# Optimization experiments

Measured on AMD Instinct MI355X. Metric: run time of the kernel, lower is better.

Reference implementation:

```python
import jax, jax.numpy as jnp
import numpy as np

B, S, HID, H, DH = 8, 4096, 1024, 16, 64


def setup_inputs() -> dict:
    key = jax.random.key(0)
    ks = jax.random.split(key, 5)
    return {
        "hidden_states": jax.random.normal(ks[0], (B, S, HID), dtype=jnp.float32),
        "attention_mask": jnp.ones((B, 1, 1, S), dtype=jnp.float32),
        "Wq": jax.random.normal(ks[1], (HID, HID), dtype=jnp.float32) * (HID ** -0.5),
        "Wk": jax.random.normal(ks[2], (HID, HID), dtype=jnp.float32) * (HID ** -0.5),
        "Wv": jax.random.normal(ks[3], (HID, HID), dtype=jnp.float32) * (HID ** -0.5),
        "att_weight": jax.random.normal(ks[4], (H, 1, DH), dtype=jnp.float32) * (DH ** -0.5),
    }


def _heads(x):
    # [B,S,HID] -> [B,H,S,DH]
    b, s, _ = x.shape
    return x.reshape(b, s, H, DH).transpose(0, 2, 1, 3)


def reference(hidden_states, attention_mask, Wq, Wk, Wv, att_weight):
    # bias-free projections (torch Linear: x @ W.T)
    q = _heads(hidden_states @ Wq.T)  # [B,H,S,DH]
    k = _heads(hidden_states @ Wk.T)
    v = _heads(hidden_states @ Wv.T)

    mask = attention_mask.transpose(0, 1, 3, 2)  # [B,1,S,1]
    aw = att_weight[:, 0, :]  # [H,DH]

    q_scores = jnp.einsum('bhsd,hd->bhs', q, aw)[..., None] * mask  # [B,H,S,1]
    k_scores = jnp.einsum('bhsd,hd->bhs', k, aw)[..., None] * mask  # [B,H,S,1]

    length = jnp.sum(mask, axis=-2, keepdims=True)            # [B,1,1,1]
    mean_value = jnp.sum(v * mask, axis=-2, keepdims=True)    # [B,H,1,DH]

    query_values = q_scores * mean_value                      # [B,H,S,DH] outer product
    key_values = jnp.einsum('bhs,bhsd->bhd', k_scores[..., 0], v)[:, :, None, :]  # [B,H,1,DH]

    ctx = (query_values + key_values) / length                # [B,H,S,DH]
    ctx = ctx.transpose(0, 2, 1, 3).reshape(ctx.shape[0], ctx.shape[2], H * DH)
    return ctx
```

## Files before the change

kernel.cpp:

```cpp
#include <hip/hip_runtime.h>

#define BB 8
#define SS 4096
#define HIDD 1024
#define HH 16
#define DHH 64

typedef __attribute__((ext_vector_type(8))) short bf16x8;
typedef __attribute__((ext_vector_type(4))) float f32x4;

static __device__ __forceinline__ unsigned short f2bf(float x) {
    union { float f; unsigned int u; } a; a.f = x;
    unsigned int r = a.u + 0x7FFFu + ((a.u >> 16) & 1u);
    return (unsigned short)(r >> 16);
}
static __device__ __forceinline__ float bf2f(unsigned short b) {
    union { unsigned int u; float f; } a; a.u = ((unsigned int)b) << 16;
    return a.f;
}

__global__ __launch_bounds__(256) void k_prep(const float* __restrict__ Wq,
                                              const float* __restrict__ Wk,
                                              const float* __restrict__ aw,
                                              unsigned short* __restrict__ bpack) {
    int k = blockIdx.x * 256 + threadIdx.x;
    int h = blockIdx.y;
    const float* W = blockIdx.z ? Wk : Wq;
    int nt = blockIdx.z;
    float acc = 0.f;
#pragma unroll
    for (int d = 0; d < DHH; ++d) {
        acc += aw[h * DHH + d] * W[(size_t)(h * DHH + d) * HIDD + k];
    }
    unsigned short hi = f2bf(acc);
    unsigned short lo = f2bf(acc - bf2f(hi));
    int kk   = k >> 5;
    int r5   = (k >> 3) & 3;
    int j    = k & 7;
    int lane = r5 * 16 + h;
    size_t baseh = ((size_t)(kk * 4 + 0 + nt) * 256 + lane * 4) * 2 + j;
    size_t basel = ((size_t)(kk * 4 + 2 + nt) * 256 + lane * 4) * 2 + j;
    bpack[baseh] = hi;
    bpack[basel] = lo;
}

#define KC 64
__global__ __launch_bounds__(256) void k_scores(const float* __restrict__ hid,
                                                const float* __restrict__ mask,
                                                const unsigned short* __restrict__ bpack,
                                                float* __restrict__ qsb,
                                                float* __restrict__ ksb) {
    __shared__ float shh[2][64 * 68];

    const int t    = threadIdx.x;
    const int lane = t & 63;
    const int wave = t >> 6;
    const int rbase = blockIdx.x * 64;
    const size_t gbase = (size_t)rbase * HIDD;

    int srow[5], scol[5];
#pragma unroll
    for (int j = 0; j < 5; ++j) {
        int f = (j < 4) ? (j * 256 + t) : (1024 + t);
        int r = f / 17;
        int c = f - r * 17;
        srow[j] = r;
        scol[j] = (c == 16) ? 0 : c;
    }
    const bool extra = (t < 64);

    auto stage = [&](int chunk, int buf) {
#pragma unroll
        for (int j = 0; j < 4; ++j) {
            const float* gp = hid + gbase + (size_t)srow[j] * HIDD
                              + chunk * KC + scol[j] * 4;
            float* lp = &shh[buf][(j * 256 + t) * 4];
            __builtin_amdgcn_global_load_lds(
                (const __attribute__((address_space(1))) void*)gp,
                (__attribute__((address_space(3))) void*)lp, 16, 0, 0);
        }
        if (extra) {
            const float* gp = hid + gbase + (size_t)srow[4] * HIDD
                              + chunk * KC + scol[4] * 4;
            float* lp = &shh[buf][(1024 + t) * 4];
            __builtin_amdgcn_global_load_lds(
                (const __attribute__((address_space(1))) void*)gp,
                (__attribute__((address_space(3))) void*)lp, 16, 0, 0);
        }
    };

    const bf16x8* bview = reinterpret_cast<const bf16x8*>(bpack);
    const int mrow = wave * 16 + (lane & 15);
    const int koff = (lane >> 4) * 8;

    f32x4 accq = {0.f, 0.f, 0.f, 0.f};
    f32x4 acck = {0.f, 0.f, 0.f, 0.f};

    stage(0, 0);

    for (int chunk = 0; chunk < HIDD / KC; ++chunk) {
        const int buf = chunk & 1;
        asm volatile("s_waitcnt vmcnt(0)" ::: "memory");
        __syncthreads();
        if (chunk + 1 < HIDD / KC) stage(chunk + 1, buf ^ 1);

#pragma unroll
        for (int kl = 0; kl < 2; ++kl) {
            const int kk = chunk * 2 + kl;
            bf16x8 bh0 = bview[(kk * 4 + 0) * 64 + lane];
            bf16x8 bh1 = bview[(kk * 4 + 1) * 64 + lane];
            bf16x8 bl0 = bview[(kk * 4 + 2) * 64 + lane];
            bf16x8 bl1 = bview[(kk * 4 + 3) * 64 + lane];

            const float* ap = &shh[buf][mrow * 68 + kl * 32 + koff];
            float4 av0 = *reinterpret_cast<const float4*>(ap);
            float4 av1 = *reinterpret_cast<const float4*>(ap + 4);
            float a[8] = {av0.x, av0.y, av0.z, av0.w, av1.x, av1.y, av1.z, av1.w};
            union { bf16x8 v; unsigned short u[8]; } Ahi, Alo;
#pragma unroll
            for (int j = 0; j < 8; ++j) {
                unsigned short hb = f2bf(a[j]);
                Ahi.u[j] = hb;
                Alo.u[j] = f2bf(a[j] - bf2f(hb));
            }

            accq = __builtin_amdgcn_mfma_f32_16x16x32_bf16(Ahi.v, bh0, accq, 0, 0, 0);
            accq = __builtin_amdgcn_mfma_f32_16x16x32_bf16(Alo.v, bh0, accq, 0, 0, 0);
            accq = __builtin_amdgcn_mfma_f32_16x16x32_bf16(Ahi.v, bl0, accq, 0, 0, 0);
            acck = __builtin_amdgcn_mfma_f32_16x16x32_bf16(Ahi.v, bh1, acck, 0, 0, 0);
            acck = __builtin_amdgcn_mfma_f32_16x16x32_bf16(Alo.v, bh1, acck, 0, 0, 0);
            acck = __builtin_amdgcn_mfma_f32_16x16x32_bf16(Ahi.v, bl1, acck, 0, 0, 0);
        }
    }

#pragma unroll
    for (int reg = 0; reg < 4; ++reg) {
        int grow = rbase + wave * 16 + (lane >> 4) * 4 + reg;
        float m = mask[grow];
        qsb[(size_t)grow * 16 + (lane & 15)] = accq[reg] * m;
        ksb[(size_t)grow * 20 + (lane & 15)] = acck[reg] * m;
        if ((lane & 15) == 0) ksb[(size_t)grow * 20 + 16] = m;
    }
}

__global__ __launch_bounds__(256) void k_ksh(const float* __restrict__ hid,
                                             const float* __restrict__ ksb,
                                             float* __restrict__ part) {
    int b  = blockIdx.y;
    int i  = threadIdx.x * 4;
    int s0 = blockIdx.x * 64;

    float4 acc[17];
#pragma unroll
    for (int c = 0; c < 17; ++c) acc[c] = make_float4(0.f, 0.f, 0.f, 0.f);

    const float* hb = hid + (size_t)(b * SS + s0) * HIDD + i;
    const float* sb = ksb + (size_t)(b * SS + s0) * 20;

#pragma unroll 4
    for (int s = 0; s < 64; ++s) {
        float4 hv = *reinterpret_cast<const float4*>(hb + (size_t)s * HIDD);
        const float* sc = sb + s * 20;
#pragma unroll
        for (int c = 0; c < 17; ++c) {
            float scv = sc[c];
            acc[c].x += scv * hv.x;
            acc[c].y += scv * hv.y;
            acc[c].z += scv * hv.z;
            acc[c].w += scv * hv.w;
        }
    }

    float* pb = part + (((size_t)blockIdx.x * 8 + b) * 17) * 1024 + i;
#pragma unroll
    for (int c = 0; c < 17; ++c) {
        *reinterpret_cast<float4*>(pb + c * 1024) = acc[c];
    }
}

__global__ __launch_bounds__(256) void k_red(const float* __restrict__ part,
                                             float* __restrict__ ksh,
                                             float* __restrict__ hsum) {
    int gid = blockIdx.x * 256 + threadIdx.x;
    int b = gid / 17408;
    int r = gid - b * 17408;
    int c = r >> 10;
    int i = r & 1023;

    float s = 0.f;
#pragma unroll 8
    for (int k = 0; k < 64; ++k)
        s += part[(((size_t)k * 8 + b) * 17 + c) * 1024 + i];

    if (c < 16) ksh[((size_t)b * 16 + c) * 1024 + i] = s;
    else        hsum[b * 1024 + i] = s;
}

__global__ __launch_bounds__(256) void k_fin(const float* __restrict__ Wv,
                                             const float* __restrict__ mask,
                                             const float* __restrict__ hsum,
                                             const float* __restrict__ ksh,
                                             float* __restrict__ mvn,
                                             float* __restrict__ kvn) {
    int b  = blockIdx.x;
    int j  = blockIdx.y * 32 + (threadIdx.x >> 3);
    int sl = threadIdx.x & 7;

    __shared__ float red[256];
    float lsum = 0.f;
    for (int s = threadIdx.x; s < SS; s += 256) lsum += mask[b * SS + s];
    red[threadIdx.x] = lsum;
    __syncthreads();
    for (int off = 128; off; off >>= 1) {
        if (threadIdx.x < off) red[threadIdx.x] += red[threadIdx.x + off];
        __syncthreads();
    }
    float invlen = 1.0f / red[0];

    int h = j >> 6;
    const float4* w4 = reinterpret_cast<const float4*>(Wv + (size_t)j * HIDD + sl * 128);
    const float4* hv = reinterpret_cast<const float4*>(hsum + b * HIDD + sl * 128);
    const float4* kv = reinterpret_cast<const float4*>(ksh + ((size_t)b * 16 + h) * HIDD + sl * 128);

    float mv = 0.f, kvv = 0.f;
#pragma unroll
    for (int c = 0; c < 32; ++c) {
        float4 w = w4[c], a = hv[c], k2 = kv[c];
        mv  += w.x * a.x  + w.y * a.y  + w.z * a.z  + w.w * a.w;
        kvv += w.x * k2.x + w.y * k2.y + w.z * k2.z + w.w * k2.w;
    }
#pragma unroll
    for (int off = 1; off < 8; off <<= 1) {
        mv  += __shfl_xor(mv, off);
        kvv += __shfl_xor(kvv, off);
    }
    if (sl == 0) {
        mvn[b * HIDD + j] = mv * invlen;
        kvn[b * HIDD + j] = kvv * invlen;
    }
}

__global__ __launch_bounds__(256) void k_out(const float* __restrict__ qsb,
                                             const float* __restrict__ mvn,
                                             const float* __restrict__ kvn,
                                             float* __restrict__ outp) {
    size_t e0 = ((size_t)blockIdx.x * 256 + threadIdx.x) * 8;
    int b   = (int)(e0 >> 22);
    int rem = (int)(e0 & ((1u << 22) - 1));
    int s   = rem >> 10;
    int j   = rem & 1023;

    float q = qsb[(size_t)(b * SS + s) * 16 + (j >> 6)];
    const float4* mv4 = reinterpret_cast<const float4*>(mvn + b * HIDD + j);
    const float4* kv4 = reinterpret_cast<const float4*>(kvn + b * HIDD + j);
    float4 m0 = mv4[0], m1 = mv4[1];
    float4 k0 = kv4[0], k1 = kv4[1];

    float4 o0, o1;
    o0.x = q * m0.x + k0.x;  o0.y = q * m0.y + k0.y;
    o0.z = q * m0.z + k0.z;  o0.w = q * m0.w + k0.w;
    o1.x = q * m1.x + k1.x;  o1.y = q * m1.y + k1.y;
    o1.z = q * m1.z + k1.z;  o1.w = q * m1.w + k1.w;

    float4* op = reinterpret_cast<float4*>(outp + e0);
    op[0] = o0;
    op[1] = o1;
}

extern "C" void kernel_launch(void* const* d_in, const int* in_sizes, int n_in,
                              void* d_out, int out_size, void* d_ws, size_t ws_size,
                              hipStream_t stream) {
    const float* hid  = (const float*)d_in[0];
    const float* mask = (const float*)d_in[1];
    const float* Wq   = (const float*)d_in[2];
    const float* Wk   = (const float*)d_in[3];
    const float* Wv   = (const float*)d_in[4];
    const float* aw   = (const float*)d_in[5];
    float* outp = (float*)d_out;

    float* ws   = (float*)d_ws;
    unsigned short* bpack = (unsigned short*)ws;
    float* qsb  = ws + 32768;
    float* ksb  = qsb + 524288;
    float* ksh  = ksb + 655360;
    float* hsum = ksh + 131072;
    float* mvn  = hsum + 8192;
    float* kvn  = mvn + 8192;
    float* part = kvn + 8192;

    k_prep  <<<dim3(4, 16, 2), 256, 0, stream>>>(Wq, Wk, aw, bpack);
    k_scores<<<dim3(512),      256, 0, stream>>>(hid, mask, bpack, qsb, ksb);
    k_ksh   <<<dim3(64, 8),    256, 0, stream>>>(hid, ksb, part);
    k_red   <<<dim3(544),      256, 0, stream>>>(part, ksh, hsum);
    k_fin   <<<dim3(8, 32),    256, 0, stream>>>(Wv, mask, hsum, ksh, mvn, kvn);
    k_out   <<<dim3(16384),    256, 0, stream>>>(qsb, mvn, kvn, outp);
}
```

Measured before the change: 349.6 us.

## Triple-buffer hidden-state staging in k_scores with partial vmcnt waits

The LDS staging of hidden-state chunks in k_scores moves from two buffers to three, so two chunks are kept in flight ahead of the compute. The loop waits with vmcnt(5) instead of vmcnt(0), letting the next chunk's loads stay outstanding while the current chunk is consumed. The extra-row loads are remapped so each wave issues them for its own 16 lanes, which keeps the per-wave outstanding-load count uniform for the counter. It costs more LDS per block, which may lower occupancy, and the exact vmcnt accounting is fragile.

```diff
diff --git a/kernel.cpp b/kernel.cpp
--- a/kernel.cpp
+++ b/kernel.cpp
@@ -45,12 +45,13 @@
 }
 
 #define KC 64
+#define NCH (HIDD / KC)
 __global__ __launch_bounds__(256) void k_scores(const float* __restrict__ hid,
                                                 const float* __restrict__ mask,
                                                 const unsigned short* __restrict__ bpack,
                                                 float* __restrict__ qsb,
                                                 float* __restrict__ ksb) {
-    __shared__ float shh[2][64 * 68];
+    __shared__ float shh[3][64 * 68];
 
     const int t    = threadIdx.x;
     const int lane = t & 63;
@@ -58,31 +59,31 @@
     const int rbase = blockIdx.x * 64;
     const size_t gbase = (size_t)rbase * HIDD;
 
-    int srow[5], scol[5];
+    int srow[5], scol[5], sslot[5];
 #pragma unroll
     for (int j = 0; j < 5; ++j) {
-        int f = (j < 4) ? (j * 256 + t) : (1024 + t);
+        int f = (j < 4) ? (j * 256 + t) : (1024 + wave * 16 + (lane & 15));
         int r = f / 17;
         int c = f - r * 17;
-        srow[j] = r;
-        scol[j] = (c == 16) ? 0 : c;
-    }
-    const bool extra = (t < 64);
+        srow[j]  = r;
+        scol[j]  = (c == 16) ? 0 : c;
+        sslot[j] = f;
+    }
 
     auto stage = [&](int chunk, int buf) {
 #pragma unroll
         for (int j = 0; j < 4; ++j) {
             const float* gp = hid + gbase + (size_t)srow[j] * HIDD
                               + chunk * KC + scol[j] * 4;
-            float* lp = &shh[buf][(j * 256 + t) * 4];
+            float* lp = &shh[buf][sslot[j] * 4];
             __builtin_amdgcn_global_load_lds(
                 (const __attribute__((address_space(1))) void*)gp,
                 (__attribute__((address_space(3))) void*)lp, 16, 0, 0);
         }
-        if (extra) {
+        if (lane < 16) {
             const float* gp = hid + gbase + (size_t)srow[4] * HIDD
                               + chunk * KC + scol[4] * 4;
-            float* lp = &shh[buf][(1024 + t) * 4];
+            float* lp = &shh[buf][sslot[4] * 4];
             __builtin_amdgcn_global_load_lds(
                 (const __attribute__((address_space(1))) void*)gp,
                 (__attribute__((address_space(3))) void*)lp, 16, 0, 0);
@@ -97,12 +98,22 @@
     f32x4 acck = {0.f, 0.f, 0.f, 0.f};
 
     stage(0, 0);
-
-    for (int chunk = 0; chunk < HIDD / KC; ++chunk) {
-        const int buf = chunk & 1;
-        asm volatile("s_waitcnt vmcnt(0)" ::: "memory");
-        __syncthreads();
-        if (chunk + 1 < HIDD / KC) stage(chunk + 1, buf ^ 1);
+    stage(1, 1);
+
+    int cbuf = 0;
+    for (int chunk = 0; chunk < NCH; ++chunk) {
+        __builtin_amdgcn_sched_barrier(0);
+        if (chunk < NCH - 1) {
+            asm volatile("s_waitcnt vmcnt(5)" ::: "memory");
+        } else {
+            asm volatile("s_waitcnt vmcnt(0)" ::: "memory");
+        }
+        __builtin_amdgcn_s_barrier();
+        __builtin_amdgcn_sched_barrier(0);
+        if (chunk + 2 < NCH) {
+            int sbuf = (cbuf == 0) ? 2 : cbuf - 1;
+            stage(chunk + 2, sbuf);
+        }
 
 #pragma unroll
         for (int kl = 0; kl < 2; ++kl) {
@@ -112,7 +123,7 @@
             bf16x8 bl0 = bview[(kk * 4 + 2) * 64 + lane];
             bf16x8 bl1 = bview[(kk * 4 + 3) * 64 + lane];
 
-            const float* ap = &shh[buf][mrow * 68 + kl * 32 + koff];
+            const float* ap = &shh[cbuf][mrow * 68 + kl * 32 + koff];
             float4 av0 = *reinterpret_cast<const float4*>(ap);
             float4 av1 = *reinterpret_cast<const float4*>(ap + 4);
             float a[8] = {av0.x, av0.y, av0.z, av0.w, av1.x, av1.y, av1.z, av1.w};
@@ -131,6 +142,7 @@
             acck = __builtin_amdgcn_mfma_f32_16x16x32_bf16(Alo.v, bh1, acck, 0, 0, 0);
             acck = __builtin_amdgcn_mfma_f32_16x16x32_bf16(Ahi.v, bl1, acck, 0, 0, 0);
         }
+        cbuf = (cbuf == 2) ? 0 : cbuf + 1;
     }
 
 #pragma unroll
```

After: 347.0 us. No clear change (-0.8%).
